# Kernel optimization log

Measured on AMD Instinct MI355X. Metric: run time of the kernel, lower is better.

Reference implementation:

```python
import jax, jax.numpy as jnp
import numpy as np

KH = KW = 3
K = KH * KW
STRIDE = 1
PAD = 1
DIL = 1
GROUPS = 1
DG = 1  # deformable_groups
CIN = 256
COUT = 256
DC = 64  # depth_channels


def conv2d(x, w, b):
    out = jax.lax.conv_general_dilated(
        x, w, (STRIDE, STRIDE), [(PAD, PAD), (PAD, PAD)],
        rhs_dilation=(DIL, DIL), dimension_numbers=('NCHW', 'OIHW', 'NCHW'))
    return out + b[None, :, None, None]


def deform_sample(x, offset, mask):
    """Modulated deformable im2col. x:[N,C,H,W], offset:[N,DG*2*K,Ho,Wo],
    mask:[N,DG*K,Ho,Wo] or None. Returns cols [N,C,K,Ho,Wo]."""
    N, C, H, W = x.shape
    Ho = (H + 2 * PAD - (DIL * (KH - 1) + 1)) // STRIDE + 1
    Wo = (W + 2 * PAD - (DIL * (KW - 1) + 1)) // STRIDE + 1
    ky, kx = jnp.meshgrid(jnp.arange(KH), jnp.arange(KW), indexing='ij')
    # base sampling grid per kernel tap: [K,Ho,Wo]
    base_y = (jnp.arange(Ho) * STRIDE - PAD)[None, :, None] + (ky.reshape(-1) * DIL)[:, None, None]
    base_x = (jnp.arange(Wo) * STRIDE - PAD)[None, None, :] + (kx.reshape(-1) * DIL)[:, None, None]
    off = offset.reshape(N, DG, K, 2, Ho, Wo)  # [...,0]=dy, [...,1]=dx (CUDA layout)
    y = base_y[None, None].astype(x.dtype) + off[:, :, :, 0]
    xx = base_x[None, None].astype(x.dtype) + off[:, :, :, 1]
    y0 = jnp.floor(y)
    x0 = jnp.floor(xx)
    ly = y - y0
    lx = xx - x0
    y0i = y0.astype(jnp.int32)
    x0i = x0.astype(jnp.int32)
    xg = x.reshape(N, DG, C // DG, H * W)

    def gather(iy, ix):
        valid = ((iy >= 0) & (iy < H) & (ix >= 0) & (ix < W)).astype(x.dtype)
        idx = (jnp.clip(iy, 0, H - 1) * W + jnp.clip(ix, 0, W - 1)).reshape(N, DG, 1, K * Ho * Wo)
        v = jnp.take_along_axis(xg, idx, axis=3).reshape(N, DG, C // DG, K, Ho, Wo)
        return v * valid[:, :, None]

    v00 = gather(y0i, x0i)
    v01 = gather(y0i, x0i + 1)
    v10 = gather(y0i + 1, x0i)
    v11 = gather(y0i + 1, x0i + 1)
    w00 = (1 - ly) * (1 - lx)
    w01 = (1 - ly) * lx
    w10 = ly * (1 - lx)
    w11 = ly * lx
    cols = (v00 * w00[:, :, None] + v01 * w01[:, :, None]
            + v10 * w10[:, :, None] + v11 * w11[:, :, None])
    if mask is not None:
        cols = cols * mask.reshape(N, DG, 1, K, Ho, Wo)
    return cols.reshape(N, C, K, Ho, Wo)


def deform_conv2d(x, offset, mask, weight, bias):
    cols = deform_sample(x, offset, mask)  # [N,C,K,Ho,Wo]
    N, C, _, Ho, Wo = cols.shape
    Cout = weight.shape[0]
    cg = C // GROUPS
    cols = cols.reshape(N, GROUPS, cg * K, Ho * Wo)
    wg = weight.reshape(GROUPS, Cout // GROUPS, cg * K)
    out = jnp.einsum('gok,ngkp->ngop', wg, cols).reshape(N, Cout, Ho, Wo)
    return out + bias[None, :, None, None]


def setup_inputs() -> dict:
    key = jax.random.key(0)
    ks = jax.random.split(key, 8)
    x = jax.random.normal(ks[0], (4, CIN, 64, 64), dtype=jnp.float32)
    depth = jax.random.normal(ks[1], (4, DC, 64, 64), dtype=jnp.float32)
    stdv = 1.0 / np.sqrt(CIN * KH * KW)
    weight = jax.random.uniform(ks[2], (COUT, CIN // GROUPS, KH, KW), minval=-stdv, maxval=stdv, dtype=jnp.float32)
    bias = jnp.zeros((COUT,), jnp.float32)
    # offset/mask convs are zero-init in the module; use small random weights
    # so the irregular gather path is actually exercised.
    off_w = 0.05 * jax.random.normal(ks[3], (DG * 2 * K, CIN + DC, KH, KW), dtype=jnp.float32)
    off_b = 0.05 * jax.random.normal(ks[4], (DG * 2 * K,), dtype=jnp.float32)
    mask_w = 0.05 * jax.random.normal(ks[5], (DG * K, DC, KH, KW), dtype=jnp.float32)
    mask_b = 0.05 * jax.random.normal(ks[6], (DG * K,), dtype=jnp.float32)
    return {"x": x, "depth": depth, "weight": weight, "bias": bias,
            "off_w": off_w, "off_b": off_b, "mask_w": mask_w, "mask_b": mask_b}


def reference(x, depth, weight, bias, off_w, off_b, mask_w, mask_b):
    # offset = conv_offset(cat(x, depth))
    offset = conv2d(jnp.concatenate([x, depth], axis=1), off_w, off_b)
    # mask = sigmoid(DeformConv(depth, offset))  (non-modulated deform conv)
    mask = jax.nn.sigmoid(deform_conv2d(depth, offset, None, mask_w, mask_b))
    # modulated deformable conv on x
    return deform_conv2d(x, offset, mask, weight, bias)
```

## Files before the change

### kernel.cpp

```cpp
#include <hip/hip_runtime.h>


typedef __bf16 bf16x8 __attribute__((ext_vector_type(8)));
typedef float f32x4 __attribute__((ext_vector_type(4)));
typedef float float2_u __attribute__((ext_vector_type(2), aligned(4)));

__device__ __forceinline__ unsigned short f2bf(float f) {
  unsigned b = __float_as_uint(f);
  return (unsigned short)((b + 0x7fffu + ((b >> 16) & 1u)) >> 16);
}

__global__ __launch_bounds__(256) void k_prep_weight(
    const float* __restrict__ w, unsigned short* __restrict__ wbf)
{
  const int i = blockIdx.x * 256 + threadIdx.x;
  wbf[i] = f2bf(w[i]);
}

__global__ __launch_bounds__(256) void k_offset_conv(
    const float* __restrict__ x, const float* __restrict__ depth,
    const float* __restrict__ off_w, const float* __restrict__ off_b,
    float* __restrict__ offs)
{
  const int seg = blockIdx.x >> 8;
  const int nh  = blockIdx.x & 255;
  const int n = nh >> 6, ho = nh & 63;
  const int tid = threadIdx.x;
  const int lane = tid & 63;
  const int wave = tid >> 6;

  float acc[18];
#pragma unroll
  for (int i = 0; i < 18; ++i) acc[i] = 0.f;

  const int c0 = __builtin_amdgcn_readfirstlane(seg * 80 + wave * 20);

  for (int ci = 0; ci < 20; ++ci) {
    const int c = c0 + ci;
    const float* p = (c < 256) ? (x + (((n << 8) + c) << 12))
                               : (depth + (((n << 6) + (c - 256)) << 12));
    const float v0 = (ho > 0)  ? p[((ho - 1) << 6) + lane] : 0.f;
    const float v1 =             p[( ho      << 6) + lane];
    const float v2 = (ho < 63) ? p[((ho + 1) << 6) + lane] : 0.f;

    float v[9];
#pragma unroll
    for (int ky = 0; ky < 3; ++ky) {
      const float r = (ky == 0) ? v0 : ((ky == 1) ? v1 : v2);
#pragma unroll
      for (int kx = 0; kx < 3; ++kx) {
        const int src = lane + kx - 1;
        const float s = __shfl(r, src & 63);
        v[ky * 3 + kx] = (src >= 0 && src < 64) ? s : 0.f;
      }
    }
    const float* wp = off_w + c * 9;
#pragma unroll
    for (int co = 0; co < 18; ++co) {
      const float* w = wp + co * 2880;
#pragma unroll
      for (int t = 0; t < 9; ++t) acc[co] += v[t] * w[t];
    }
  }

  __shared__ float red[4][18][64];
#pragma unroll
  for (int co = 0; co < 18; ++co) red[wave][co][lane] = acc[co];
  __syncthreads();
  for (int o = tid; o < 18 * 64; o += 256) {
    const int co = o >> 6, wo = o & 63;
    float s = red[0][co][wo] + red[1][co][wo] + red[2][co][wo] + red[3][co][wo];
    if (seg == 0) s += off_b[co];
    atomicAdd(&offs[((n * 18 + co) << 12) + (ho << 6) + wo], s);
  }
}

__global__ __launch_bounds__(512) void k_mask_conv(
    const float* __restrict__ depth, const float* __restrict__ offs,
    const float* __restrict__ mask_w, const float* __restrict__ mask_b,
    float* __restrict__ mask)
{
  const int n  = blockIdx.x >> 6;
  const int ho = blockIdx.x & 63;
  const int tid  = threadIdx.x;
  const int lane = tid & 63;
  const int wave = tid >> 6;
  const int wo = lane;

  int i00[9], i01[9], i10[9], i11[9];
  float cw00[9], cw01[9], cw10[9], cw11[9];
  const float* op = offs + ((n * 18) << 12) + (ho << 6) + wo;
#pragma unroll
  for (int k = 0; k < 9; ++k) {
    const float dy = op[(2 * k) << 12];
    const float dx = op[(2 * k + 1) << 12];
    const float yy = (float)(ho - 1 + k / 3) + dy;
    const float xx = (float)(wo - 1 + k % 3) + dx;
    const float y0f = floorf(yy), x0f = floorf(xx);
    const float ly = yy - y0f, lx = xx - x0f;
    const int y0 = (int)y0f, x0 = (int)x0f;
    const int y0c = min(max(y0, 0), 63),     x0c = min(max(x0, 0), 63);
    const int y1c = min(max(y0 + 1, 0), 63), x1c = min(max(x0 + 1, 0), 63);
    const float fy0 = (y0 >= 0 && y0 < 64) ? 1.f : 0.f;
    const float fy1 = (y0 >= -1 && y0 < 63) ? 1.f : 0.f;
    const float fx0 = (x0 >= 0 && x0 < 64) ? 1.f : 0.f;
    const float fx1 = (x0 >= -1 && x0 < 63) ? 1.f : 0.f;
    i00[k] = (y0c << 6) + x0c;  i01[k] = (y0c << 6) + x1c;
    i10[k] = (y1c << 6) + x0c;  i11[k] = (y1c << 6) + x1c;
    cw00[k] = (1.f - ly) * (1.f - lx) * fy0 * fx0;
    cw01[k] = (1.f - ly) * lx * fy0 * fx1;
    cw10[k] = ly * (1.f - lx) * fy1 * fx0;
    cw11[k] = ly * lx * fy1 * fx1;
  }

  float acc[9];
#pragma unroll
  for (int i = 0; i < 9; ++i) acc[i] = 0.f;

  const int cbase = __builtin_amdgcn_readfirstlane(wave * 8);
  for (int cc = 0; cc < 8; ++cc) {
    const int c = cbase + cc;
    const float* p = depth + (((n << 6) + c) << 12);
    float val[9];
#pragma unroll
    for (int k = 0; k < 9; ++k) {
      val[k] = p[i00[k]] * cw00[k] + p[i01[k]] * cw01[k] +
               p[i10[k]] * cw10[k] + p[i11[k]] * cw11[k];
    }
    const float* wp = mask_w + c * 9;
#pragma unroll
    for (int co = 0; co < 9; ++co) {
#pragma unroll
      for (int k = 0; k < 9; ++k) acc[co] += val[k] * wp[co * 576 + k];
    }
  }

  __shared__ float red[8][9][64];
#pragma unroll
  for (int co = 0; co < 9; ++co) red[wave][co][lane] = acc[co];
  __syncthreads();
  for (int o = tid; o < 9 * 64; o += 512) {
    const int co = o >> 6, w2 = o & 63;
    float s = mask_b[co];
#pragma unroll
    for (int w = 0; w < 8; ++w) s += red[w][co][w2];
    mask[((n * 9 + co) << 12) + (ho << 6) + w2] = 1.f / (1.f + expf(-s));
  }
}

__global__ __launch_bounds__(512, 2) void k_deform_gemm(
    const float* __restrict__ x, const float* __restrict__ offs,
    const float* __restrict__ mask, const unsigned short* __restrict__ wbf,
    const float* __restrict__ bias, float* __restrict__ out)
{
  __shared__ __align__(16) unsigned short Bs[2][64][72];
  __shared__ float4 pwT[9][64];
  __shared__ int2   piT[9][64];

  const int tid = threadIdx.x;
  const int b    = blockIdx.x;
  const int xcd  = b & 7, slot = b >> 3;
  const int n    = xcd >> 1;
  const int ho0  = ((xcd & 1) << 5) + slot;
  const int pxb  = ho0 << 6;
  const int pxg0 = (n << 12) + pxb;

  for (int e = tid; e < 576; e += 512) {
    const int tap = e >> 6, pl = e & 63;
    const int pxg = pxg0 + pl;
    const int wo = pl;
    const float dy = offs[((n * 18 + 2 * tap) << 12) + pxb + pl];
    const float dx = offs[((n * 18 + 2 * tap + 1) << 12) + pxb + pl];
    const float m  = mask[((n * 9 + tap) << 12) + pxb + pl];
    (void)pxg;
    const float yy = (float)(ho0 - 1 + tap / 3) + dy;
    const float xx = (float)(wo - 1 + tap % 3) + dx;
    const float y0f = floorf(yy), x0f = floorf(xx);
    const float ly = yy - y0f, lx = xx - x0f;
    const int y0 = (int)y0f, x0 = (int)x0f;
    const int y0c = min(max(y0, 0), 63);
    const int y1c = min(max(y0 + 1, 0), 63);
    const float fy0 = (y0 >= 0 && y0 < 64) ? 1.f : 0.f;
    const float fy1 = (y0 >= -1 && y0 < 63) ? 1.f : 0.f;
    const int x0c = min(max(x0, 0), 63);
    const int x1c = min(max(x0 + 1, 0), 63);
    const int bx  = min(max(x0, 0), 62);
    const float vx0 = (x0 >= 0 && x0 < 64) ? 1.f : 0.f;
    const float vx1 = (x0 >= -1 && x0 < 63) ? 1.f : 0.f;
    const float wl = (1.f - lx) * vx0 * ((x0c == bx) ? 1.f : 0.f)
                   + lx * vx1 * ((x1c == bx) ? 1.f : 0.f);
    const float wr = (1.f - lx) * vx0 * ((x0c == bx + 1) ? 1.f : 0.f)
                   + lx * vx1 * ((x1c == bx + 1) ? 1.f : 0.f);
    const float a0 = (1.f - ly) * fy0 * m;
    const float a1 = ly * fy1 * m;
    pwT[tap][pl] = make_float4(wl * a0, wr * a0, wl * a1, wr * a1);
    piT[tap][pl] = make_int2((((y0c << 6) + bx) << 2), (((y1c << 6) + bx) << 2));
  }
  __syncthreads();

  const int pxl = tid & 63;
  const int oct = tid >> 6;
  const float* xn = x + ((long)(n << 8) << 12);

  auto sample = [&](int kc, int buf) {
    const int kk0 = kc + (oct << 3);
    int c = (int)(((unsigned)kk0 * 7282u) >> 16);
    int tap = kk0 - 9 * c;
    const char* p = (const char*)(xn + (c << 12));
    __align__(16) unsigned short v[8];
#pragma unroll
    for (int j = 0; j < 8; ++j) {
      const float4 w = pwT[tap][pxl];
      const int2 ii  = piT[tap][pxl];
      const float2_u pa = *(const float2_u*)(p + ii.x);
      const float2_u pb = *(const float2_u*)(p + ii.y);
      v[j] = f2bf(pa.x * w.x + pa.y * w.y + pb.x * w.z + pb.y * w.w);
      if (++tap == 9) { tap = 0; p += 16384; }
    }
    *(int4*)&Bs[buf][pxl][oct << 3] = *(const int4*)v;
  };

  f32x4 acc[2][4];
#pragma unroll
  for (int mt = 0; mt < 2; ++mt)
#pragma unroll
    for (int nt = 0; nt < 4; ++nt)
#pragma unroll
      for (int r = 0; r < 4; ++r) acc[mt][nt][r] = 0.f;

  sample(0, 0);
  __syncthreads();

  const int wv   = oct;
  const int lane = tid & 63;
  const int mrow = lane & 15;
  const int koct = lane >> 4;

  for (int ic = 0; ic < 36; ++ic) {
    const int kc = ic << 6;
    bf16x8 af[2][2];
#pragma unroll
    for (int mt = 0; mt < 2; ++mt)
#pragma unroll
      for (int ks = 0; ks < 2; ++ks) {
        const int row = (wv << 5) + (mt << 4) + mrow;
        const int col = kc + (ks << 5) + (koct << 3);
        af[mt][ks] = *(const bf16x8*)(wbf + row * 2304 + col);
      }

    if (ic + 1 < 36) sample((ic + 1) << 6, (ic + 1) & 1);

    const int buf = ic & 1;
#pragma unroll
    for (int ks = 0; ks < 2; ++ks)
#pragma unroll
      for (int nt = 0; nt < 4; ++nt) {
        const bf16x8 bfr =
            *(const bf16x8*)&Bs[buf][(nt << 4) + mrow][(ks << 5) + (koct << 3)];
        acc[0][nt] = __builtin_amdgcn_mfma_f32_16x16x32_bf16(af[0][ks], bfr,
                                                             acc[0][nt], 0, 0, 0);
        acc[1][nt] = __builtin_amdgcn_mfma_f32_16x16x32_bf16(af[1][ks], bfr,
                                                             acc[1][nt], 0, 0, 0);
      }
    __syncthreads();
  }

#pragma unroll
  for (int mt = 0; mt < 2; ++mt)
#pragma unroll
    for (int nt = 0; nt < 4; ++nt)
#pragma unroll
      for (int r = 0; r < 4; ++r) {
        const int co = (wv << 5) + (mt << 4) + ((lane >> 4) << 2) + r;
        const int pxg = pxb + (nt << 4) + (lane & 15);
        out[(((n << 8) + co) << 12) + pxg] = acc[mt][nt][r] + bias[co];
      }
}

extern "C" void kernel_launch(void* const* d_in, const int* in_sizes, int n_in,
                              void* d_out, int out_size, void* d_ws, size_t ws_size,
                              hipStream_t stream) {
  const float* x      = (const float*)d_in[0];
  const float* depth  = (const float*)d_in[1];
  const float* weight = (const float*)d_in[2];
  const float* bias   = (const float*)d_in[3];
  const float* off_w  = (const float*)d_in[4];
  const float* off_b  = (const float*)d_in[5];
  const float* mask_w = (const float*)d_in[6];
  const float* mask_b = (const float*)d_in[7];
  float* out = (float*)d_out;

  float* offs = (float*)d_ws;
  float* mask = offs + 294912;
  unsigned short* wbf = (unsigned short*)(mask + 147456);

  hipMemsetAsync(offs, 0, 294912 * sizeof(float), stream);
  k_prep_weight<<<2304, 256, 0, stream>>>(weight, wbf);
  k_offset_conv<<<1024, 256, 0, stream>>>(x, depth, off_w, off_b, offs);
  k_mask_conv<<<256, 512, 0, stream>>>(depth, offs, mask_w, mask_b, mask);
  k_deform_gemm<<<256, 512, 0, stream>>>(x, offs, mask, wbf, bias, out);
}
```

Measured before the change: 281.3 us.

## Fuse offset and mask convs; split-K deform GEMM with fixed-point atomics

Merges the offset conv and mask conv into one kernel per output row. The offset reduction now runs inside a 512-thread block, which drops the offset atomics and the memset, and the mask sampling reuses the precomputed bilinear pair-load tables from shared memory. The deform GEMM is split four ways along K (1024 blocks instead of 256, launch bounds raised to 8) to raise occupancy. Partial results are accumulated with integer atomics in fixed-point, so the sums stay deterministic, and a finalize kernel converts them back to float. The cost is extra atomic traffic, a zeroing pass over the output, and quantisation or overflow risk from the 2^22 fixed-point scale.

After: 343.7 us. 22.2% more time.

```diff
diff --git a/kernel.cpp b/kernel.cpp
--- a/kernel.cpp
+++ b/kernel.cpp
@@ -4,6 +4,9 @@
 typedef __bf16 bf16x8 __attribute__((ext_vector_type(8)));
 typedef float f32x4 __attribute__((ext_vector_type(4)));
 typedef float float2_u __attribute__((ext_vector_type(2), aligned(4)));
+
+#define FIXSCALE 4194304.0f
+#define FIXINV   2.38418579101562e-7f
 
 __device__ __forceinline__ unsigned short f2bf(float f) {
   unsigned b = __float_as_uint(f);
@@ -17,15 +20,21 @@
   wbf[i] = f2bf(w[i]);
 }
 
-__global__ __launch_bounds__(256) void k_offset_conv(
+__global__ __launch_bounds__(512) void k_offmask(
     const float* __restrict__ x, const float* __restrict__ depth,
     const float* __restrict__ off_w, const float* __restrict__ off_b,
-    float* __restrict__ offs)
+    const float* __restrict__ mask_w, const float* __restrict__ mask_b,
+    float* __restrict__ offs, float* __restrict__ mask)
 {
-  const int seg = blockIdx.x >> 8;
-  const int nh  = blockIdx.x & 255;
-  const int n = nh >> 6, ho = nh & 63;
-  const int tid = threadIdx.x;
+  __shared__ float  redA[8][18][64];
+  __shared__ float  offsRow[18][64];
+  __shared__ float4 qw[9][64];
+  __shared__ int2   qi[9][64];
+  __shared__ float  redB[8][9][64];
+
+  const int n  = blockIdx.x >> 6;
+  const int ho = blockIdx.x & 63;
+  const int tid  = threadIdx.x;
   const int lane = tid & 63;
   const int wave = tid >> 6;
 
@@ -33,9 +42,8 @@
 #pragma unroll
   for (int i = 0; i < 18; ++i) acc[i] = 0.f;
 
-  const int c0 = __builtin_amdgcn_readfirstlane(seg * 80 + wave * 20);
-
-  for (int ci = 0; ci < 20; ++ci) {
+  const int c0 = __builtin_amdgcn_readfirstlane(wave * 40);
+  for (int ci = 0; ci < 40; ++ci) {
     const int c = c0 + ci;
     const float* p = (c < 256) ? (x + (((n << 8) + c) << 12))
                                : (depth + (((n << 6) + (c - 256)) << 12));
@@ -62,96 +70,84 @@
       for (int t = 0; t < 9; ++t) acc[co] += v[t] * w[t];
     }
   }
-
-  __shared__ float red[4][18][64];
-#pragma unroll
-  for (int co = 0; co < 18; ++co) red[wave][co][lane] = acc[co];
-  __syncthreads();
-  for (int o = tid; o < 18 * 64; o += 256) {
+#pragma unroll
+  for (int co = 0; co < 18; ++co) redA[wave][co][lane] = acc[co];
+  __syncthreads();
+  for (int o = tid; o < 18 * 64; o += 512) {
     const int co = o >> 6, wo = o & 63;
-    float s = red[0][co][wo] + red[1][co][wo] + red[2][co][wo] + red[3][co][wo];
-    if (seg == 0) s += off_b[co];
-    atomicAdd(&offs[((n * 18 + co) << 12) + (ho << 6) + wo], s);
-  }
-}
-
-__global__ __launch_bounds__(512) void k_mask_conv(
-    const float* __restrict__ depth, const float* __restrict__ offs,
-    const float* __restrict__ mask_w, const float* __restrict__ mask_b,
-    float* __restrict__ mask)
-{
-  const int n  = blockIdx.x >> 6;
-  const int ho = blockIdx.x & 63;
-  const int tid  = threadIdx.x;
-  const int lane = tid & 63;
-  const int wave = tid >> 6;
-  const int wo = lane;
-
-  int i00[9], i01[9], i10[9], i11[9];
-  float cw00[9], cw01[9], cw10[9], cw11[9];
-  const float* op = offs + ((n * 18) << 12) + (ho << 6) + wo;
-#pragma unroll
-  for (int k = 0; k < 9; ++k) {
-    const float dy = op[(2 * k) << 12];
-    const float dx = op[(2 * k + 1) << 12];
-    const float yy = (float)(ho - 1 + k / 3) + dy;
-    const float xx = (float)(wo - 1 + k % 3) + dx;
+    float s = off_b[co];
+#pragma unroll
+    for (int w = 0; w < 8; ++w) s += redA[w][co][wo];
+    offsRow[co][wo] = s;
+    offs[((n * 18 + co) << 12) + (ho << 6) + wo] = s;
+  }
+  __syncthreads();
+
+  for (int e = tid; e < 576; e += 512) {
+    const int tap = e >> 6, pl = e & 63;
+    const float dy = offsRow[2 * tap][pl];
+    const float dx = offsRow[2 * tap + 1][pl];
+    const float yy = (float)(ho - 1 + tap / 3) + dy;
+    const float xx = (float)(pl - 1 + tap % 3) + dx;
     const float y0f = floorf(yy), x0f = floorf(xx);
     const float ly = yy - y0f, lx = xx - x0f;
     const int y0 = (int)y0f, x0 = (int)x0f;
-    const int y0c = min(max(y0, 0), 63),     x0c = min(max(x0, 0), 63);
-    const int y1c = min(max(y0 + 1, 0), 63), x1c = min(max(x0 + 1, 0), 63);
+    const int y0c = min(max(y0, 0), 63);
+    const int y1c = min(max(y0 + 1, 0), 63);
     const float fy0 = (y0 >= 0 && y0 < 64) ? 1.f : 0.f;
     const float fy1 = (y0 >= -1 && y0 < 63) ? 1.f : 0.f;
-    const float fx0 = (x0 >= 0 && x0 < 64) ? 1.f : 0.f;
-    const float fx1 = (x0 >= -1 && x0 < 63) ? 1.f : 0.f;
-    i00[k] = (y0c << 6) + x0c;  i01[k] = (y0c << 6) + x1c;
-    i10[k] = (y1c << 6) + x0c;  i11[k] = (y1c << 6) + x1c;
-    cw00[k] = (1.f - ly) * (1.f - lx) * fy0 * fx0;
-    cw01[k] = (1.f - ly) * lx * fy0 * fx1;
-    cw10[k] = ly * (1.f - lx) * fy1 * fx0;
-    cw11[k] = ly * lx * fy1 * fx1;
-  }
-
-  float acc[9];
-#pragma unroll
-  for (int i = 0; i < 9; ++i) acc[i] = 0.f;
+    const int x0c = min(max(x0, 0), 63);
+    const int x1c = min(max(x0 + 1, 0), 63);
+    const int bx  = min(max(x0, 0), 62);
+    const float vx0 = (x0 >= 0 && x0 < 64) ? 1.f : 0.f;
+    const float vx1 = (x0 >= -1 && x0 < 63) ? 1.f : 0.f;
+    const float wl = (1.f - lx) * vx0 * ((x0c == bx) ? 1.f : 0.f)
+                   + lx * vx1 * ((x1c == bx) ? 1.f : 0.f);
+    const float wr = (1.f - lx) * vx0 * ((x0c == bx + 1) ? 1.f : 0.f)
+                   + lx * vx1 * ((x1c == bx + 1) ? 1.f : 0.f);
+    const float a0 = (1.f - ly) * fy0;
+    const float a1 = ly * fy1;
+    qw[tap][pl] = make_float4(wl * a0, wr * a0, wl * a1, wr * a1);
+    qi[tap][pl] = make_int2((((y0c << 6) + bx) << 2), (((y1c << 6) + bx) << 2));
+  }
+  __syncthreads();
+
+  float accB[9];
+#pragma unroll
+  for (int i = 0; i < 9; ++i) accB[i] = 0.f;
 
   const int cbase = __builtin_amdgcn_readfirstlane(wave * 8);
   for (int cc = 0; cc < 8; ++cc) {
     const int c = cbase + cc;
-    const float* p = depth + (((n << 6) + c) << 12);
-    float val[9];
-#pragma unroll
-    for (int k = 0; k < 9; ++k) {
-      val[k] = p[i00[k]] * cw00[k] + p[i01[k]] * cw01[k] +
-               p[i10[k]] * cw10[k] + p[i11[k]] * cw11[k];
+    const char* p = (const char*)(depth + (((n << 6) + c) << 12));
+    const float* wp = mask_w + c * 9;
+#pragma unroll
+    for (int tap = 0; tap < 9; ++tap) {
+      const float4 w4 = qw[tap][lane];
+      const int2 ii   = qi[tap][lane];
+      const float2_u pa = *(const float2_u*)(p + ii.x);
+      const float2_u pb = *(const float2_u*)(p + ii.y);
+      const float val = pa.x * w4.x + pa.y * w4.y + pb.x * w4.z + pb.y * w4.w;
+#pragma unroll
+      for (int co = 0; co < 9; ++co) accB[co] += val * wp[co * 576 + tap];
     }
-    const float* wp = mask_w + c * 9;
-#pragma unroll
-    for (int co = 0; co < 9; ++co) {
-#pragma unroll
-      for (int k = 0; k < 9; ++k) acc[co] += val[k] * wp[co * 576 + k];
-    }
-  }
-
-  __shared__ float red[8][9][64];
-#pragma unroll
-  for (int co = 0; co < 9; ++co) red[wave][co][lane] = acc[co];
+  }
+#pragma unroll
+  for (int co = 0; co < 9; ++co) redB[wave][co][lane] = accB[co];
   __syncthreads();
   for (int o = tid; o < 9 * 64; o += 512) {
     const int co = o >> 6, w2 = o & 63;
     float s = mask_b[co];
 #pragma unroll
-    for (int w = 0; w < 8; ++w) s += red[w][co][w2];
+    for (int w = 0; w < 8; ++w) s += redB[w][co][w2];
     mask[((n * 9 + co) << 12) + (ho << 6) + w2] = 1.f / (1.f + expf(-s));
   }
 }
 
-__global__ __launch_bounds__(512, 2) void k_deform_gemm(
+__global__ __launch_bounds__(512, 8) void k_deform_gemm(
     const float* __restrict__ x, const float* __restrict__ offs,
     const float* __restrict__ mask, const unsigned short* __restrict__ wbf,
-    const float* __restrict__ bias, float* __restrict__ out)
+    const float* __restrict__ bias, int* __restrict__ outi)
 {
   __shared__ __align__(16) unsigned short Bs[2][64][72];
   __shared__ float4 pwT[9][64];
@@ -159,22 +155,21 @@
 
   const int tid = threadIdx.x;
   const int b    = blockIdx.x;
-  const int xcd  = b & 7, slot = b >> 3;
+  const int xcd  = b & 7;
+  const int s    = b >> 3;
+  const int kq   = s & 3;
+  const int rs   = s >> 2;
   const int n    = xcd >> 1;
-  const int ho0  = ((xcd & 1) << 5) + slot;
+  const int ho0  = ((xcd & 1) << 5) + rs;
   const int pxb  = ho0 << 6;
-  const int pxg0 = (n << 12) + pxb;
 
   for (int e = tid; e < 576; e += 512) {
     const int tap = e >> 6, pl = e & 63;
-    const int pxg = pxg0 + pl;
-    const int wo = pl;
     const float dy = offs[((n * 18 + 2 * tap) << 12) + pxb + pl];
     const float dx = offs[((n * 18 + 2 * tap + 1) << 12) + pxb + pl];
     const float m  = mask[((n * 9 + tap) << 12) + pxb + pl];
-    (void)pxg;
     const float yy = (float)(ho0 - 1 + tap / 3) + dy;
-    const float xx = (float)(wo - 1 + tap % 3) + dx;
+    const float xx = (float)(pl - 1 + tap % 3) + dx;
     const float y0f = floorf(yy), x0f = floorf(xx);
     const float ly = yy - y0f, lx = xx - x0f;
     const int y0 = (int)y0f, x0 = (int)x0f;
@@ -228,16 +223,17 @@
 #pragma unroll
       for (int r = 0; r < 4; ++r) acc[mt][nt][r] = 0.f;
 
-  sample(0, 0);
-  __syncthreads();
-
+  const int kb = kq * 576;
+  sample(kb, 0);
+  __syncthreads();
+
+  const int lane = tid & 63;
   const int wv   = oct;
-  const int lane = tid & 63;
   const int mrow = lane & 15;
   const int koct = lane >> 4;
 
-  for (int ic = 0; ic < 36; ++ic) {
-    const int kc = ic << 6;
+  for (int ic = 0; ic < 9; ++ic) {
+    const int kc = kb + (ic << 6);
     bf16x8 af[2][2];
 #pragma unroll
     for (int mt = 0; mt < 2; ++mt)
@@ -248,7 +244,7 @@
         af[mt][ks] = *(const bf16x8*)(wbf + row * 2304 + col);
       }
 
-    if (ic + 1 < 36) sample((ic + 1) << 6, (ic + 1) & 1);
+    if (ic + 1 < 9) sample(kb + ((ic + 1) << 6), (ic + 1) & 1);
 
     const int buf = ic & 1;
 #pragma unroll
@@ -273,8 +269,23 @@
       for (int r = 0; r < 4; ++r) {
         const int co = (wv << 5) + (mt << 4) + ((lane >> 4) << 2) + r;
         const int pxg = pxb + (nt << 4) + (lane & 15);
-        out[(((n << 8) + co) << 12) + pxg] = acc[mt][nt][r] + bias[co];
+        float v = acc[mt][nt][r];
+        if (kq == 0) v += bias[co];
+        const int iv = __float2int_rn(v * FIXSCALE);
+        atomicAdd(&outi[(((n << 8) + co) << 12) + pxg], iv);
       }
+}
+
+__global__ __launch_bounds__(256) void k_finalize(float* __restrict__ out)
+{
+  const int i = (blockIdx.x * 256 + threadIdx.x) << 2;
+  int4 iv = *(const int4*)((const int*)out + i);
+  float4 fv;
+  fv.x = (float)iv.x * FIXINV;
+  fv.y = (float)iv.y * FIXINV;
+  fv.z = (float)iv.z * FIXINV;
+  fv.w = (float)iv.w * FIXINV;
+  *(float4*)(out + i) = fv;
 }
 
 extern "C" void kernel_launch(void* const* d_in, const int* in_sizes, int n_in,
@@ -294,9 +305,10 @@
   float* mask = offs + 294912;
   unsigned short* wbf = (unsigned short*)(mask + 147456);
 
-  hipMemsetAsync(offs, 0, 294912 * sizeof(float), stream);
+  hipMemsetAsync(out, 0, (size_t)out_size * sizeof(float), stream);
   k_prep_weight<<<2304, 256, 0, stream>>>(weight, wbf);
-  k_offset_conv<<<1024, 256, 0, stream>>>(x, depth, off_w, off_b, offs);
-  k_mask_conv<<<256, 512, 0, stream>>>(depth, offs, mask_w, mask_b, mask);
-  k_deform_gemm<<<256, 512, 0, stream>>>(x, offs, mask, wbf, bias, out);
-}
+  k_offmask<<<256, 512, 0, stream>>>(x, depth, off_w, off_b, mask_w, mask_b,
+                                     offs, mask);
+  k_deform_gemm<<<1024, 512, 0, stream>>>(x, offs, mask, wbf, bias, (int*)out);
+  k_finalize<<<out_size / 1024, 256, 0, stream>>>(out);
+}
```
